# Performance work log

Measured on AMD Instinct MI355X. Metric: run time of the kernel, lower is better.

## Reference

```python
import jax, jax.numpy as jnp
import numpy as np
from jax import lax

B, T, D, U = 64, 512, 1024, 128


def setup_inputs() -> dict:
    key = jax.random.key(0)
    k1, k2, k3, k4 = jax.random.split(key, 4)
    inputs = jax.random.normal(k1, (B, T, D), dtype=jnp.float32)
    kernel = jax.random.normal(k2, (D, U), dtype=jnp.float32) * (1.0 / np.sqrt(D))
    bias = jnp.zeros((U,), dtype=jnp.float32)
    chain_kernel = jax.random.normal(k4, (U, U), dtype=jnp.float32) * 0.1
    return {"inputs": inputs, "kernel": kernel, "bias": bias, "chain_kernel": chain_kernel}


def _viterbi_decode(logits, chain_kernel):
    # logits: [B, T, U]; chain_kernel[i, j] = score of transition i -> j
    state0 = logits[:, 0]                      # [B, U]
    pots = jnp.swapaxes(logits[:, 1:], 0, 1)   # [T-1, B, U]

    def fwd_step(state, pot_t):
        # scores[b, i, j] = state[b, i] + chain[i, j]
        scores = state[:, :, None] + chain_kernel[None, :, :]
        backptr = jnp.argmax(scores, axis=1)           # [B, U] int
        new_state = pot_t + jnp.max(scores, axis=1)    # [B, U]
        return new_state, backptr

    final_state, backptrs = lax.scan(fwd_step, state0, pots)  # backptrs: [T-1, B, U]
    last_tag = jnp.argmax(final_state, axis=-1)               # [B]

    def back_step(tag, bp_t):
        prev = jnp.take_along_axis(bp_t, tag[:, None], axis=1)[:, 0]
        return prev, prev

    # reverse scan: tags_rev[t] = best tag at position t, for t = 0..T-2
    _, tags_rev = lax.scan(back_step, last_tag, backptrs, reverse=True)
    tags = jnp.concatenate([tags_rev, last_tag[None]], axis=0)  # [T, B]
    return jnp.swapaxes(tags, 0, 1)                             # [B, T]


def reference(inputs, kernel, bias, chain_kernel):
    # _dense_layer: linear activation(inputs @ kernel + bias)
    logits = jnp.einsum('btd,du->btu', inputs, kernel) + bias
    # mask=None -> nwords = T for every sequence (full-length decode)
    pred_ids = _viterbi_decode(logits, chain_kernel)
    return pred_ids.astype(jnp.float32)
```

## Files before the change

### kernel.cpp

```cpp
#include <hip/hip_runtime.h>

#define BB 64
#define TT 512
#define DD 1024
#define UU 128

#define GBM 128
#define GBK 64

__global__ __launch_bounds__(256, 1) void gemm_kernel(const float* __restrict__ A,
                                                      const float* __restrict__ W,
                                                      const float* __restrict__ bias,
                                                      float* __restrict__ C) {
    __shared__ __align__(16) float As[GBK][GBM];
    __shared__ __align__(16) float Ws[GBK][UU];

    const int tid = threadIdx.x;
    const int mi = tid >> 4;
    const int ni = tid & 15;
    const int row0 = blockIdx.x * GBM;

    const int ac = tid & 15;
    const int ar = tid >> 4;
    const int asw = (ac & 7) << 2;

    float acc[8][8] = {};
    float4 pa[8], pw[8];

#define GLOAD(k0)                                                                  \
    {                                                                              \
        _Pragma("unroll")                                                          \
        for (int p = 0; p < 8; ++p)                                                \
            pa[p] = *(const float4*)&A[(size_t)(row0 + ar + 16 * p) * DD + (k0) + ac * 4]; \
        _Pragma("unroll")                                                          \
        for (int q = 0; q < 8; ++q) {                                              \
            const int f = tid + 256 * q;                                           \
            pw[q] = *(const float4*)&W[(size_t)((k0) + (f >> 5)) * UU + (f & 31) * 4]; \
        }                                                                          \
    }

#define GSTORE                                                                     \
    {                                                                              \
        _Pragma("unroll")                                                          \
        for (int p = 0; p < 8; ++p) {                                              \
            const int rs = (ar + 16 * p) ^ asw;                                    \
            As[ac * 4 + 0][rs] = pa[p].x;                                          \
            As[ac * 4 + 1][rs] = pa[p].y;                                          \
            As[ac * 4 + 2][rs] = pa[p].z;                                          \
            As[ac * 4 + 3][rs] = pa[p].w;                                          \
        }                                                                          \
        _Pragma("unroll")                                                          \
        for (int q = 0; q < 8; ++q) {                                              \
            const int f = tid + 256 * q;                                           \
            *(float4*)&Ws[f >> 5][(f & 31) * 4] = pw[q];                           \
        }                                                                          \
    }

#define GCOMPUTE                                                                   \
    {                                                                              \
        _Pragma("unroll 4")                                                        \
        for (int k = 0; k < GBK; ++k) {                                            \
            const int sw = ((k >> 2) & 7) << 2;                                    \
            const float4 a0 = *(const float4*)&As[k][(mi * 8) ^ sw];               \
            const float4 a1 = *(const float4*)&As[k][(mi * 8 + 4) ^ sw];           \
            const float4 w0 = *(const float4*)&Ws[k][ni * 4];                      \
            const float4 w1 = *(const float4*)&Ws[k][64 + ni * 4];                 \
            const float a[8] = {a0.x, a0.y, a0.z, a0.w, a1.x, a1.y, a1.z, a1.w};   \
            const float w[8] = {w0.x, w0.y, w0.z, w0.w, w1.x, w1.y, w1.z, w1.w};   \
            _Pragma("unroll")                                                      \
            for (int i = 0; i < 8; ++i)                                            \
                _Pragma("unroll")                                                  \
                for (int j = 0; j < 8; ++j) acc[i][j] = fmaf(a[i], w[j], acc[i][j]); \
        }                                                                          \
    }

    GLOAD(0);
    GSTORE;
    __syncthreads();
    for (int k0 = GBK; k0 < DD; k0 += GBK) {
        GLOAD(k0);
        GCOMPUTE;
        __syncthreads();
        GSTORE;
        __syncthreads();
    }
    GCOMPUTE;

    const float4 b0 = *(const float4*)&bias[ni * 4];
    const float4 b1 = *(const float4*)&bias[64 + ni * 4];
#pragma unroll
    for (int i = 0; i < 8; ++i) {
        const int row = row0 + mi * 8 + i;
        float4 o0, o1;
        o0.x = acc[i][0] + b0.x; o0.y = acc[i][1] + b0.y;
        o0.z = acc[i][2] + b0.z; o0.w = acc[i][3] + b0.w;
        o1.x = acc[i][4] + b1.x; o1.y = acc[i][5] + b1.y;
        o1.z = acc[i][6] + b1.z; o1.w = acc[i][7] + b1.w;
        *(float4*)&C[(size_t)row * UU + ni * 4] = o0;
        *(float4*)&C[(size_t)row * UU + 64 + ni * 4] = o1;
    }
}

#define DPPI(x, ctrl) __builtin_amdgcn_mov_dpp((x), (ctrl), 0xF, 0xF, true)
#define DPPF(x, ctrl) __int_as_float(DPPI(__float_as_int(x), (ctrl)))

__device__ __forceinline__ float fmax3(float a, float b, float c) {
    float d;
    asm("v_max3_f32 %0, %1, %2, %3" : "=v"(d) : "v"(a), "v"(b), "v"(c));
    return d;
}
__device__ __forceinline__ float max16(const float* s) {
    const float g0 = fmax3(s[0], s[1], s[2]);
    const float g1 = fmax3(s[3], s[4], s[5]);
    const float g2 = fmax3(s[6], s[7], s[8]);
    const float g3 = fmax3(s[9], s[10], s[11]);
    const float g4 = fmax3(s[12], s[13], s[14]);
    return fmaxf(fmax3(g0, g1, g2), fmax3(g3, g4, s[15]));
}

__device__ __forceinline__ int SP16(int v) { return v + ((v >> 4) << 2); }

__global__ __launch_bounds__(1024, 1) void fwdbwd_kernel(float* __restrict__ lgst,
                                                         const float* __restrict__ chain,
                                                         float* __restrict__ out) {
    __shared__ __align__(16) float st[2][160];
    __shared__ __align__(16) float pot_lds[64][UU];
    __shared__ __align__(16) float hist[32][UU];

    const bool isBwd = blockIdx.x >= BB;
    const int b = isBwd ? (blockIdx.x - BB) : blockIdx.x;
    const int tid = threadIdx.x;
    const int u = tid >> 3;
    const int h = tid & 7;

    float* lg = lgst + (size_t)b * TT * UU;
    const float4* lg4 = (const float4*)lg;
    float4* pot4 = (float4*)pot_lds;
    const float4* hist4 = (const float4*)hist;

    float cr[16];
    if (!isBwd) {
#pragma unroll
        for (int j = 0; j < 16; ++j) cr[j] = chain[(size_t)(16 * h + j) * UU + u];
        for (int f = tid; f < 2048; f += 1024) pot4[f] = lg4[f];
        if (tid < UU) {
            const float v = lg[tid];
            st[0][SP16(tid)] = v;
            hist[0][tid] = v;
        }
    } else {
#pragma unroll
        for (int j = 0; j < 16; ++j) cr[j] = chain[(size_t)u * UU + 16 * h + j];
        for (int f = tid; f < 2048; f += 1024) pot4[f] = lg4[448 * 32 + f];
        if (tid < UU) {
            const float v = lg[(size_t)511 * UU + tid];
            st[0][SP16(tid)] = v;
            hist[31][tid] = v;
        }
    }
    __syncthreads();

    if (!isBwd) {
        auto step = [&](int tt, const float* stS, float* stD) {
            if ((tt & 15) == 0 && tid < 512) {
                const int r0 = tt - 16;
                ((float4*)&lg[r0 * UU])[tid] = hist4[((r0 & 31) << 5) + tid];
            }
            if ((tt & 31) == 1 && tt > 1 && tt + 31 < 256) {
                const int f0 = (tt + 31) * 32 + tid;
                pot4[f0 & 2047] = lg4[f0];
            }
            const float4* sbp = (const float4*)(stS + 20 * h);
            const float4 sv0 = sbp[0], sv1 = sbp[1], sv2 = sbp[2], sv3 = sbp[3];
            const float a[16] = {sv0.x, sv0.y, sv0.z, sv0.w, sv1.x, sv1.y, sv1.z, sv1.w,
                                 sv2.x, sv2.y, sv2.z, sv2.w, sv3.x, sv3.y, sv3.z, sv3.w};
            float s[16];
#pragma unroll
            for (int j = 0; j < 16; ++j) s[j] = a[j] + cr[j];
            float m = max16(s);
            m = fmaxf(m, DPPF(m, 0xB1));
            m = fmaxf(m, DPPF(m, 0x4E));
            m = fmaxf(m, DPPF(m, 0x104));
            if (h == 0) {
                const float ns = pot_lds[tt & 63][u] + m;
                stD[SP16(u)] = ns;
                hist[tt & 31][u] = ns;
            }
            __syncthreads();
        };
        for (int t = 1; t < 255; t += 2) {
            step(t, st[0], st[1]);
            step(t + 1, st[1], st[0]);
        }
        step(255, st[0], st[1]);
        if (tid < 512) ((float4*)&lg[240 * UU])[tid] = hist4[(16 << 5) + tid];
    } else {
        auto stepB = [&](int t, const float* stS, float* stD) {
            if ((t & 15) == 15 && tid < 512) {
                ((float4*)&lg[(t + 1) * UU])[tid] = hist4[(((t + 1) & 31) << 5) + tid];
            }
            if ((t & 31) == 31 && t >= 319) {
                const int f0 = (t - 63) * 32 + tid;
                pot4[f0 & 2047] = lg4[f0];
            }
            const float4* sbp = (const float4*)(stS + 20 * h);
            const float4 sv0 = sbp[0], sv1 = sbp[1], sv2 = sbp[2], sv3 = sbp[3];
            const float a[16] = {sv0.x, sv0.y, sv0.z, sv0.w, sv1.x, sv1.y, sv1.z, sv1.w,
                                 sv2.x, sv2.y, sv2.z, sv2.w, sv3.x, sv3.y, sv3.z, sv3.w};
            float s[16];
#pragma unroll
            for (int j = 0; j < 16; ++j) s[j] = a[j] + cr[j];
            float m = max16(s);
            m = fmaxf(m, DPPF(m, 0xB1));
            m = fmaxf(m, DPPF(m, 0x4E));
            m = fmaxf(m, DPPF(m, 0x104));
            if (h == 0) {
                if (t >= 256) {
                    const float ns = pot_lds[t & 63][u] + m;
                    stD[SP16(u)] = ns;
                    hist[t & 31][u] = ns;
                } else {
                    out[(size_t)b * TT + u] = m;
                }
            }
            __syncthreads();
        };
        for (int t = 510; t > 255; t -= 2) {
            stepB(t, st[0], st[1]);
            stepB(t - 1, st[1], st[0]);
        }
    }
}

#define MERGE2(bv, ba, ctrl)                                                      \
    {                                                                             \
        const float ov_ = DPPF((bv), ctrl); const int oa_ = DPPI((ba), ctrl);     \
        const bool tk_ = (ov_ > (bv)) || (ov_ == (bv) && oa_ < (ba));             \
        (bv) = tk_ ? ov_ : (bv); (ba) = tk_ ? oa_ : (ba);                         \
    }

__global__ __launch_bounds__(512) void ptr_kernel(const float* __restrict__ st_g,
                                                  const float* __restrict__ chain,
                                                  unsigned char* __restrict__ bp_g) {
    const int blk = blockIdx.x;
    const int b = blk >> 3;
    const int c = blk & 7;
    const int tid = threadIdx.x;
    const int g = tid >> 3;
    const int h = tid & 7;
    const int base = 16 * h;
    const bool isUp = (c >= 4);

    float cr0[16], cr1[16];
    if (!isUp) {
#pragma unroll
        for (int j = 0; j < 16; ++j) {
            cr0[j] = chain[(size_t)(base + j) * UU + 2 * g];
            cr1[j] = chain[(size_t)(base + j) * UU + 2 * g + 1];
        }
    } else {
#pragma unroll
        for (int j = 0; j < 16; ++j) {
            cr0[j] = chain[(size_t)(2 * g) * UU + base + j];
            cr1[j] = chain[(size_t)(2 * g + 1) * UU + base + j];
        }
    }

    const float* stb = st_g + (size_t)b * TT * UU;
    const int t0 = (c == 0) ? 1 : c * 64;
    const int t1 = c * 64 + 64;

    for (int t = t0; t < t1; ++t) {
        const int srow = isUp ? t : (t - 1);
        const float4* sp = (const float4*)(stb + (size_t)srow * UU + base);
        const float4 sv0 = sp[0], sv1 = sp[1], sv2 = sp[2], sv3 = sp[3];
        const float a[16] = {sv0.x, sv0.y, sv0.z, sv0.w, sv1.x, sv1.y, sv1.z, sv1.w,
                             sv2.x, sv2.y, sv2.z, sv2.w, sv3.x, sv3.y, sv3.z, sv3.w};

        float bv0, bv1;
        int ba0, ba1;
        {
            float vA = a[0] + cr0[0]; int iA = base;
            float vB = a[8] + cr0[8]; int iB = base + 8;
#pragma unroll
            for (int i = 1; i < 8; ++i) {
                const float tA = a[i] + cr0[i];
                const bool gA = tA > vA; vA = gA ? tA : vA; iA = gA ? base + i : iA;
                const float tB = a[8 + i] + cr0[8 + i];
                const bool gB = tB > vB; vB = gB ? tB : vB; iB = gB ? base + 8 + i : iB;
            }
            const bool gg = vB > vA;
            bv0 = gg ? vB : vA; ba0 = gg ? iB : iA;
        }
        {
            float vA = a[0] + cr1[0]; int iA = base;
            float vB = a[8] + cr1[8]; int iB = base + 8;
#pragma unroll
            for (int i = 1; i < 8; ++i) {
                const float tA = a[i] + cr1[i];
                const bool gA = tA > vA; vA = gA ? tA : vA; iA = gA ? base + i : iA;
                const float tB = a[8 + i] + cr1[8 + i];
                const bool gB = tB > vB; vB = gB ? tB : vB; iB = gB ? base + 8 + i : iB;
            }
            const bool gg = vB > vA;
            bv1 = gg ? vB : vA; ba1 = gg ? iB : iA;
        }
        MERGE2(bv0, ba0, 0xB1);  MERGE2(bv1, ba1, 0xB1);
        MERGE2(bv0, ba0, 0x4E);  MERGE2(bv1, ba1, 0x4E);
        MERGE2(bv0, ba0, 0x104); MERGE2(bv1, ba1, 0x104);

        if (h < 2) {
            const int v = 2 * g + h;
            bp_g[((size_t)b * TT + t) * UU + v] = (unsigned char)(h ? ba1 : ba0);
        }
    }
}

__global__ __launch_bounds__(512) void backtrace_kernel(const float* __restrict__ st_g,
                                                        const unsigned char* __restrict__ bp_g,
                                                        float* __restrict__ out) {
    __shared__ unsigned char bp[TT][UU];
    __shared__ unsigned char segmap[8][128];
    __shared__ int entryT[8];
    __shared__ int tags_i[TT];
    __shared__ int y255_s;

    const int b = blockIdx.x;
    const int tid = threadIdx.x;

    {
        const uint4* src = (const uint4*)(bp_g + (size_t)b * TT * UU);
        uint4* dst = (uint4*)bp;
#pragma unroll
        for (int i = 0; i < 8; ++i) dst[tid + 512 * i] = src[tid + 512 * i];
    }
    if (tid < 64) {
        const float* fw = st_g + ((size_t)b * TT + 255) * UU;
        const float* bw = out + (size_t)b * TT;
        float bv = fw[tid] + bw[tid];
        int bi = tid;
        const float v2 = fw[tid + 64] + bw[tid + 64];
        if (v2 > bv) { bv = v2; bi = tid + 64; }
#pragma unroll
        for (int d = 1; d < 64; d <<= 1) {
            const float ov = __shfl_xor(bv, d, 64);
            const int oi = __shfl_xor(bi, d, 64);
            if (ov > bv || (ov == bv && oi < bi)) { bv = ov; bi = oi; }
        }
        if (tid == 0) y255_s = bi;
    }
    __syncthreads();

    for (int w = tid; w < 8 * 128; w += 512) {
        const int seg = w >> 7;
        int tg = w & 127;
        if (seg < 4) {
            const int E = (seg == 3) ? 255 : 64 * (seg + 1);
            for (int t = E; t > 64 * seg; --t) tg = bp[t][tg];
        } else {
            const int B = 255 + 64 * (seg - 4);
            for (int r = B + 1; r <= B + 64; ++r) tg = bp[r][tg];
        }
        segmap[seg][w & 127] = (unsigned char)tg;
    }
    __syncthreads();

    if (tid == 0) {
        const int y255 = y255_s;
        entryT[3] = y255;
        entryT[2] = segmap[3][y255];
        entryT[1] = segmap[2][entryT[2]];
        entryT[0] = segmap[1][entryT[1]];
        entryT[4] = y255;
        entryT[5] = segmap[4][entryT[4]];
        entryT[6] = segmap[5][entryT[5]];
        entryT[7] = segmap[6][entryT[6]];
    }
    __syncthreads();

    if (tid < 8) {
        const int seg = tid;
        int tg = entryT[seg];
        if (seg < 4) {
            const int E = (seg == 3) ? 255 : 64 * (seg + 1);
            if (seg == 3) tags_i[255] = tg;
            for (int t = E; t > 64 * seg; --t) {
                tg = bp[t][tg];
                tags_i[t - 1] = tg;
            }
        } else {
            const int B = 255 + 64 * (seg - 4);
            for (int r = B + 1; r <= B + 64; ++r) {
                tg = bp[r][tg];
                tags_i[r] = tg;
            }
        }
    }
    __syncthreads();

    out[(size_t)b * TT + tid] = (float)tags_i[tid];
}

extern "C" void kernel_launch(void* const* d_in, const int* in_sizes, int n_in,
                              void* d_out, int out_size, void* d_ws, size_t ws_size,
                              hipStream_t stream) {
    const float* inputs = (const float*)d_in[0];
    const float* kern   = (const float*)d_in[1];
    const float* bias   = (const float*)d_in[2];
    const float* chain  = (const float*)d_in[3];

    float* logits_st = (float*)d_ws;
    unsigned char* bp = (unsigned char*)d_ws + (size_t)BB * TT * UU * 4;
    float* out = (float*)d_out;

    gemm_kernel<<<dim3((BB * TT) / GBM), dim3(256), 0, stream>>>(inputs, kern, bias, logits_st);
    fwdbwd_kernel<<<dim3(2 * BB), dim3(1024), 0, stream>>>(logits_st, chain, out);
    ptr_kernel<<<dim3(BB * 8), dim3(512), 0, stream>>>(logits_st, chain, bp);
    backtrace_kernel<<<dim3(BB), dim3(512), 0, stream>>>(logits_st, bp, out);
}
```

Before: 340.0 us.

## Split GEMM along K into two partials and fuse the reduction into the Viterbi kernel

The logits GEMM now runs 512 blocks instead of 256, each covering half of the K dimension, and writes two partial outputs. The forward/backward Viterbi kernel adds the two partials plus the bias when it loads potentials and writes the summed logits back for the later kernels. This is meant to fill more compute units in the GEMM (256 blocks underfill the device) while avoiding a separate reduction kernel. In exchange it costs extra workspace and extra global reads in the serial Viterbi kernel, and it relies on the write-back covering every row before ptr_kernel reads it.

```diff
diff --git a/kernel.cpp b/kernel.cpp
--- a/kernel.cpp
+++ b/kernel.cpp
@@ -5,62 +5,67 @@
 #define DD 1024
 #define UU 128
 
-#define GBM 128
-#define GBK 64
-
-__global__ __launch_bounds__(256, 1) void gemm_kernel(const float* __restrict__ A,
+#define KS_BM 128
+#define KS_BK 32
+
+__global__ __launch_bounds__(256, 2) void gemm_ksplit(const float* __restrict__ A,
                                                       const float* __restrict__ W,
-                                                      const float* __restrict__ bias,
-                                                      float* __restrict__ C) {
-    __shared__ __align__(16) float As[GBK][GBM];
-    __shared__ __align__(16) float Ws[GBK][UU];
-
-    const int tid = threadIdx.x;
+                                                      float* __restrict__ P0,
+                                                      float* __restrict__ P1) {
+    __shared__ __align__(16) float As[KS_BK][KS_BM];
+    __shared__ __align__(16) float Ws[KS_BK][UU];
+
+    const int tid  = threadIdx.x;
+    const int tile = blockIdx.x & 255;
+    const int ks   = blockIdx.x >> 8;
+    const int row0 = tile * KS_BM;
+    const int kbase = ks * 512;
+    float* P = ks ? P1 : P0;
+
     const int mi = tid >> 4;
     const int ni = tid & 15;
-    const int row0 = blockIdx.x * GBM;
-
-    const int ac = tid & 15;
-    const int ar = tid >> 4;
-    const int asw = (ac & 7) << 2;
+    const int ac = tid & 7;
+    const int ar = tid >> 3;
+    const int asw = ac << 2;
 
     float acc[8][8] = {};
-    float4 pa[8], pw[8];
-
-#define GLOAD(k0)                                                                  \
+    float4 pa[4];
+
+#define KS_GLOADA(k0)                                                              \
     {                                                                              \
         _Pragma("unroll")                                                          \
-        for (int p = 0; p < 8; ++p)                                                \
-            pa[p] = *(const float4*)&A[(size_t)(row0 + ar + 16 * p) * DD + (k0) + ac * 4]; \
-        _Pragma("unroll")                                                          \
-        for (int q = 0; q < 8; ++q) {                                              \
-            const int f = tid + 256 * q;                                           \
-            pw[q] = *(const float4*)&W[(size_t)((k0) + (f >> 5)) * UU + (f & 31) * 4]; \
-        }                                                                          \
-    }
-
-#define GSTORE                                                                     \
+        for (int p = 0; p < 4; ++p)                                                \
+            pa[p] = *(const float4*)&A[(size_t)(row0 + ar + 32 * p) * DD + kbase + (k0) + ac * 4]; \
+    }
+
+#define KS_GSTOREA                                                                 \
     {                                                                              \
         _Pragma("unroll")                                                          \
-        for (int p = 0; p < 8; ++p) {                                              \
-            const int rs = (ar + 16 * p) ^ asw;                                    \
+        for (int p = 0; p < 4; ++p) {                                              \
+            const int rs = (ar + 32 * p) ^ asw;                                    \
             As[ac * 4 + 0][rs] = pa[p].x;                                          \
             As[ac * 4 + 1][rs] = pa[p].y;                                          \
             As[ac * 4 + 2][rs] = pa[p].z;                                          \
             As[ac * 4 + 3][rs] = pa[p].w;                                          \
         }                                                                          \
+    }
+
+#define KS_WSTAGE(k0)                                                              \
+    {                                                                              \
         _Pragma("unroll")                                                          \
-        for (int q = 0; q < 8; ++q) {                                              \
+        for (int q = 0; q < 4; ++q) {                                              \
             const int f = tid + 256 * q;                                           \
-            *(float4*)&Ws[f >> 5][(f & 31) * 4] = pw[q];                           \
+            const int kk = f >> 5;                                                 \
+            const int nn = (f & 31) * 4;                                           \
+            *(float4*)&Ws[kk][nn] = *(const float4*)&W[(size_t)(kbase + (k0) + kk) * UU + nn]; \
         }                                                                          \
     }
 
-#define GCOMPUTE                                                                   \
+#define KS_COMPUTE                                                                 \
     {                                                                              \
         _Pragma("unroll 4")                                                        \
-        for (int k = 0; k < GBK; ++k) {                                            \
-            const int sw = ((k >> 2) & 7) << 2;                                    \
+        for (int k = 0; k < KS_BK; ++k) {                                          \
+            const int sw = (k >> 2) << 2;                                          \
             const float4 a0 = *(const float4*)&As[k][(mi * 8) ^ sw];               \
             const float4 a1 = *(const float4*)&As[k][(mi * 8 + 4) ^ sw];           \
             const float4 w0 = *(const float4*)&Ws[k][ni * 4];                      \
@@ -74,30 +79,28 @@
         }                                                                          \
     }
 
-    GLOAD(0);
-    GSTORE;
-    __syncthreads();
-    for (int k0 = GBK; k0 < DD; k0 += GBK) {
-        GLOAD(k0);
-        GCOMPUTE;
+    KS_GLOADA(0);
+    KS_GSTOREA;
+    KS_WSTAGE(0);
+    __syncthreads();
+    for (int k0 = KS_BK; k0 < 512; k0 += KS_BK) {
+        KS_GLOADA(k0);
+        KS_COMPUTE;
         __syncthreads();
-        GSTORE;
+        KS_GSTOREA;
+        KS_WSTAGE(k0);
         __syncthreads();
     }
-    GCOMPUTE;
-
-    const float4 b0 = *(const float4*)&bias[ni * 4];
-    const float4 b1 = *(const float4*)&bias[64 + ni * 4];
+    KS_COMPUTE;
+
 #pragma unroll
     for (int i = 0; i < 8; ++i) {
         const int row = row0 + mi * 8 + i;
         float4 o0, o1;
-        o0.x = acc[i][0] + b0.x; o0.y = acc[i][1] + b0.y;
-        o0.z = acc[i][2] + b0.z; o0.w = acc[i][3] + b0.w;
-        o1.x = acc[i][4] + b1.x; o1.y = acc[i][5] + b1.y;
-        o1.z = acc[i][6] + b1.z; o1.w = acc[i][7] + b1.w;
-        *(float4*)&C[(size_t)row * UU + ni * 4] = o0;
-        *(float4*)&C[(size_t)row * UU + 64 + ni * 4] = o1;
+        o0.x = acc[i][0]; o0.y = acc[i][1]; o0.z = acc[i][2]; o0.w = acc[i][3];
+        o1.x = acc[i][4]; o1.y = acc[i][5]; o1.z = acc[i][6]; o1.w = acc[i][7];
+        *(float4*)&P[(size_t)row * UU + ni * 4] = o0;
+        *(float4*)&P[(size_t)row * UU + 64 + ni * 4] = o1;
     }
 }
 
@@ -120,7 +123,9 @@
 
 __device__ __forceinline__ int SP16(int v) { return v + ((v >> 4) << 2); }
 
-__global__ __launch_bounds__(1024, 1) void fwdbwd_kernel(float* __restrict__ lgst,
+__global__ __launch_bounds__(1024, 1) void fwdbwd_kernel(float* __restrict__ P0,
+                                                         const float* __restrict__ P1,
+                                                         const float* __restrict__ bias,
                                                          const float* __restrict__ chain,
                                                          float* __restrict__ out) {
     __shared__ __align__(16) float st[2][160];
@@ -133,27 +138,36 @@
     const int u = tid >> 3;
     const int h = tid & 7;
 
-    float* lg = lgst + (size_t)b * TT * UU;
+    float* lg = P0 + (size_t)b * TT * UU;
+    const float* p1 = P1 + (size_t)b * TT * UU;
     const float4* lg4 = (const float4*)lg;
+    const float4* p14 = (const float4*)p1;
+    const float4 bv4 = ((const float4*)bias)[tid & 31];
     float4* pot4 = (float4*)pot_lds;
     const float4* hist4 = (const float4*)hist;
 
+#define POTSUM(f)                                                                  \
+    ({ const float4 x_ = lg4[(f)]; const float4 y_ = p14[(f)];                     \
+       float4 r_; r_.x = x_.x + y_.x + bv4.x; r_.y = x_.y + y_.y + bv4.y;          \
+       r_.z = x_.z + y_.z + bv4.z; r_.w = x_.w + y_.w + bv4.w; r_; })
+
     float cr[16];
     if (!isBwd) {
 #pragma unroll
         for (int j = 0; j < 16; ++j) cr[j] = chain[(size_t)(16 * h + j) * UU + u];
-        for (int f = tid; f < 2048; f += 1024) pot4[f] = lg4[f];
+        for (int f = tid; f < 2048; f += 1024) pot4[f] = POTSUM(f);
         if (tid < UU) {
-            const float v = lg[tid];
+            const float v = lg[tid] + p1[tid] + bias[tid];
             st[0][SP16(tid)] = v;
             hist[0][tid] = v;
         }
     } else {
 #pragma unroll
         for (int j = 0; j < 16; ++j) cr[j] = chain[(size_t)u * UU + 16 * h + j];
-        for (int f = tid; f < 2048; f += 1024) pot4[f] = lg4[448 * 32 + f];
+        for (int f = tid; f < 2048; f += 1024) pot4[f] = POTSUM(448 * 32 + f);
         if (tid < UU) {
-            const float v = lg[(size_t)511 * UU + tid];
+            const size_t idx = (size_t)511 * UU + tid;
+            const float v = lg[idx] + p1[idx] + bias[tid];
             st[0][SP16(tid)] = v;
             hist[31][tid] = v;
         }
@@ -168,7 +182,7 @@
             }
             if ((tt & 31) == 1 && tt > 1 && tt + 31 < 256) {
                 const int f0 = (tt + 31) * 32 + tid;
-                pot4[f0 & 2047] = lg4[f0];
+                pot4[f0 & 2047] = POTSUM(f0);
             }
             const float4* sbp = (const float4*)(stS + 20 * h);
             const float4 sv0 = sbp[0], sv1 = sbp[1], sv2 = sbp[2], sv3 = sbp[3];
@@ -201,7 +215,7 @@
             }
             if ((t & 31) == 31 && t >= 319) {
                 const int f0 = (t - 63) * 32 + tid;
-                pot4[f0 & 2047] = lg4[f0];
+                pot4[f0 & 2047] = POTSUM(f0);
             }
             const float4* sbp = (const float4*)(stS + 20 * h);
             const float4 sv0 = sbp[0], sv1 = sbp[1], sv2 = sbp[2], sv3 = sbp[3];
@@ -409,12 +423,15 @@
     const float* bias   = (const float*)d_in[2];
     const float* chain  = (const float*)d_in[3];
 
-    float* logits_st = (float*)d_ws;
-    unsigned char* bp = (unsigned char*)d_ws + (size_t)BB * TT * UU * 4;
+    const size_t LG = (size_t)BB * TT * UU * 4;
+    const size_t BP = (size_t)BB * TT * UU;
+    float* P0 = (float*)d_ws;
+    unsigned char* bp = (unsigned char*)d_ws + LG;
+    float* P1 = (float*)((unsigned char*)d_ws + LG + BP);
     float* out = (float*)d_out;
 
-    gemm_kernel<<<dim3((BB * TT) / GBM), dim3(256), 0, stream>>>(inputs, kern, bias, logits_st);
-    fwdbwd_kernel<<<dim3(2 * BB), dim3(1024), 0, stream>>>(logits_st, chain, out);
-    ptr_kernel<<<dim3(BB * 8), dim3(512), 0, stream>>>(logits_st, chain, bp);
-    backtrace_kernel<<<dim3(BB), dim3(512), 0, stream>>>(logits_st, bp, out);
-}
+    gemm_ksplit<<<dim3(512), dim3(256), 0, stream>>>(inputs, kern, P0, P1);
+    fwdbwd_kernel<<<dim3(2 * BB), dim3(1024), 0, stream>>>(P0, P1, bias, chain, out);
+    ptr_kernel<<<dim3(BB * 8), dim3(512), 0, stream>>>(P0, chain, bp);
+    backtrace_kernel<<<dim3(BB), dim3(512), 0, stream>>>(P0, bp, out);
+}
```

Result: faster. 308.7 us (-9.2%).
